# Kernel tuning notes

Measured on AMD Instinct MI355X. Metric: run time of the kernel, lower is better.

## Reference

```python
import jax, jax.numpy as jnp
import numpy as np

K = 30           # k for kNN graph in each DynamicEdgeConv
NS = 0.2         # LeakyReLU negative_slope used by the repo's MLP
N = 16384        # number of points
E = 262144       # number of candidate edges
IN_CH = 3


def _glorot(key, shape):
    fan_in, fan_out = shape
    s = jnp.sqrt(6.0 / (fan_in + fan_out))
    return jax.random.uniform(key, shape, minval=-s, maxval=s, dtype=jnp.float32)


def setup_inputs() -> dict:
    key = jax.random.key(0)
    ks = jax.random.split(key, 8)
    x = jax.random.normal(ks[0], (N, IN_CH), dtype=jnp.float32)
    edge_index = jax.random.randint(ks[1], (2, E), 0, N)
    return {
        "x": x,
        "edge_index": edge_index,
        # conv1: MLP([2*in_ch, 64])
        "W1": _glorot(ks[2], (2 * IN_CH, 64)), "b1": jnp.zeros((64,), jnp.float32),
        # conv2/conv3: MLP([2*64, 64])
        "W2": _glorot(ks[3], (128, 64)), "b2": jnp.zeros((64,), jnp.float32),
        "W3": _glorot(ks[4], (128, 64)), "b3": jnp.zeros((64,), jnp.float32),
        # edge head W = MLP([2*64, 64, 1])
        "Wh1": _glorot(ks[5], (128, 64)), "bh1": jnp.zeros((64,), jnp.float32),
        "Wh2": _glorot(ks[6], (64, 1)), "bh2": jnp.zeros((1,), jnp.float32),
    }


def _knn_idx(x, k):
    # kNN in feature space (includes self, as PyG's knn(x, x, k) does)
    sq = jnp.sum(x * x, axis=1)                       # [N]
    d = sq[:, None] + sq[None, :] - 2.0 * (x @ x.T)   # [N, N] squared distances
    return jax.lax.top_k(-d, k)[1]                    # [N, k]


def _edge_conv(x, W, b):
    # DynamicEdgeConv: per-neighbor MLP on [x_i, x_j - x_i], max aggregation
    idx = _knn_idx(x, K)                              # [N, K]
    xj = x[idx]                                       # [N, K, C]
    xi = jnp.broadcast_to(x[:, None, :], xj.shape)
    feat = jnp.concatenate([xi, xj - xi], axis=-1)    # [N, K, 2C]
    h = jax.nn.leaky_relu(feat @ W + b, NS)           # [N, K, 64]
    return jnp.max(h, axis=1)                         # [N, 64]


def reference(x, edge_index, W1, b1, W2, b2, W3, b3, Wh1, bh1, Wh2, bh2):
    x = _edge_conv(x, W1, b1)
    x = _edge_conv(x, W2, b2)
    x = _edge_conv(x, W3, b3)
    # torch.sort(edge_index, dim=0) canonicalizes each column (i<=j).
    # unique + inverse-gather is mathematically the identity on the per-edge
    # outputs (duplicate columns produce identical rows), so we compute the
    # edge head directly on the sorted (canonical) edges.
    v = jnp.sort(edge_index, axis=0)                  # [2, E]
    e = jnp.concatenate([x[v[0]], x[v[1]]], axis=1)   # [E, 128]
    h = jax.nn.leaky_relu(e @ Wh1 + bh1, NS)          # [E, 64]
    out = h @ Wh2 + bh2                               # [E, 1]
    return jax.nn.sigmoid(out).reshape(-1)            # [E]
```

## Files before the change

kernel.cpp:

```cpp
#include <hip/hip_runtime.h>
#include <cmath>

typedef __attribute__((ext_vector_type(8))) short bf16x8;
typedef __attribute__((ext_vector_type(4))) float f32x4;

constexpr int N_PTS = 16384;
constexpr int KK    = 30;
constexpr int NEDGE = 262144;
constexpr float NS  = 0.2f;
constexpr int S_SL  = 16;
constexpr int M_L   = 8;
constexpr int CPQ   = S_SL * 4 * M_L;

__device__ inline short f2bf_rne(float f) {
  unsigned u = __float_as_uint(f);
  unsigned r = (u + 0x7fffu + ((u >> 16) & 1u)) >> 16;
  return (short)r;
}

#define CEA(a, i, j) { unsigned lo_ = a[i] < a[j] ? a[i] : a[j]; \
                       unsigned hi_ = a[i] < a[j] ? a[j] : a[i]; \
                       a[i] = lo_; a[j] = hi_; }
#define SORT8(a) \
  CEA(a,0,1) CEA(a,2,3) CEA(a,4,5) CEA(a,6,7) \
  CEA(a,0,2) CEA(a,1,3) CEA(a,4,6) CEA(a,5,7) \
  CEA(a,1,2) CEA(a,5,6) \
  CEA(a,0,4) CEA(a,1,5) CEA(a,2,6) CEA(a,3,7) \
  CEA(a,2,4) CEA(a,3,5) \
  CEA(a,1,2) CEA(a,3,4) CEA(a,5,6)
#define MERGE8(kd, nk) \
  { _Pragma("unroll") for (int t_ = 0; t_ < 8; ++t_) { \
      unsigned v_ = nk[7 - t_]; kd[t_] = kd[t_] < v_ ? kd[t_] : v_; } } \
  CEA(kd,0,4) CEA(kd,1,5) CEA(kd,2,6) CEA(kd,3,7) \
  CEA(kd,0,2) CEA(kd,1,3) CEA(kd,4,6) CEA(kd,5,7) \
  CEA(kd,0,1) CEA(kd,2,3) CEA(kd,4,5) CEA(kd,6,7)

#define CEP(i, j) { bool c_ = (d[i] < d[j]) || (d[i] == d[j] && id[i] < id[j]); \
  float dl_ = c_ ? d[i] : d[j], dh_ = c_ ? d[j] : d[i]; \
  int   il_ = c_ ? id[i] : id[j], ih_ = c_ ? id[j] : id[i]; \
  d[i] = dl_; d[j] = dh_; id[i] = il_; id[j] = ih_; }
#define SORTP8() \
  CEP(0,1) CEP(2,3) CEP(4,5) CEP(6,7) \
  CEP(0,2) CEP(1,3) CEP(4,6) CEP(5,7) \
  CEP(1,2) CEP(5,6) \
  CEP(0,4) CEP(1,5) CEP(2,6) CEP(3,7) \
  CEP(2,4) CEP(3,5) \
  CEP(1,2) CEP(3,4) CEP(5,6)

#define ROR_ADD(x, N) \
  { float t_ = __int_as_float(__builtin_amdgcn_update_dpp( \
        0, __float_as_int(x), 0x120 + (N), 0xF, 0xF, 0)); (x) += t_; }

__global__ __launch_bounds__(256) void sq3(const float* __restrict__ X,
                                           float* __restrict__ sqv) {
  int p = blockIdx.x * 256 + threadIdx.x;
  float s = 0.f;
#pragma unroll
  for (int c = 0; c < 3; ++c) { float v = X[(size_t)p * 3 + c]; s = fmaf(v, v, s); }
  sqv[p] = s;
}

template<int C, int CP>
__global__ __launch_bounds__(256) void sqhi(const float* __restrict__ X,
    float* __restrict__ sqv, short* __restrict__ Xh) {
  int p = blockIdx.x * 256 + threadIdx.x;
  float s = 0.f;
#pragma unroll
  for (int c = 0; c < C; ++c) {
    float v = X[(size_t)p * C + c];
    s = fmaf(v, v, s);
    Xh[(size_t)p * CP + c] = f2bf_rne(v);
  }
#pragma unroll
  for (int c = C; c < CP; ++c) Xh[(size_t)p * CP + c] = 0;
  sqv[p] = s;
}

__global__ __launch_bounds__(256) void knn_scan3(
    const float* __restrict__ X, const float* __restrict__ sqv,
    unsigned short* __restrict__ cand) {
  const int q = blockIdx.x * 256 + threadIdx.x;
  const int slice = blockIdx.y;
  const int c0 = slice * 1024;
  const float x0 = X[(size_t)q * 3 + 0];
  const float x1 = X[(size_t)q * 3 + 1];
  const float x2 = X[(size_t)q * 3 + 2];

  unsigned kq0[8], kq1[8], kq2[8], kq3[8];
#pragma unroll
  for (int t = 0; t < 8; ++t) { kq0[t]=0xFFFFFFFFu; kq1[t]=0xFFFFFFFFu;
                                kq2[t]=0xFFFFFFFFu; kq3[t]=0xFFFFFFFFu; }

#define SCAN_QTR(kd, QO) \
  for (int t = 0; t < 256; t += 8) { \
    unsigned nk[8]; \
    _Pragma("unroll") for (int u = 0; u < 8; ++u) { \
      const int j = c0 + (QO) * 256 + t + u; \
      float dj = fmaf(x0, X[(size_t)j*3+0], fmaf(x1, X[(size_t)j*3+1], x2 * X[(size_t)j*3+2])); \
      float key = fmaf(dj, -2.f, sqv[j]); \
      unsigned uu = __float_as_uint(key); \
      uu ^= ((unsigned)((int)uu >> 31)) | 0x80000000u; \
      nk[u] = (uu & 0xFFFFFF00u) | (unsigned)(t + u); \
    } \
    SORT8(nk) MERGE8(kd, nk) \
  }
  SCAN_QTR(kq0, 0)
  SCAN_QTR(kq1, 1)
  SCAN_QTR(kq2, 2)
  SCAN_QTR(kq3, 3)
#undef SCAN_QTR

  unsigned short* o = cand + (size_t)q * CPQ + slice * 32;
#pragma unroll
  for (int t = 0; t < 8; ++t) {
    o[t]      = (unsigned short)(c0 +   0 + (int)(kq0[t] & 0xFFu));
    o[8 + t]  = (unsigned short)(c0 + 256 + (int)(kq1[t] & 0xFFu));
    o[16 + t] = (unsigned short)(c0 + 512 + (int)(kq2[t] & 0xFFu));
    o[24 + t] = (unsigned short)(c0 + 768 + (int)(kq3[t] & 0xFFu));
  }
}

template<int KT>
__global__ __launch_bounds__(256) void knn_pass1(
    const short* __restrict__ Xh, const float* __restrict__ sqv,
    unsigned short* __restrict__ cand) {
  constexpr int CP = KT * 32;
  const int tid  = threadIdx.x;
  const int lane = tid & 63;
  const int wv   = tid >> 6;
  const int col  = lane & 15;
  const int quad = lane >> 4;
  const int qb   = blockIdx.x * 256 + wv * 64 + col;
  const int slice = blockIdx.y;
  const int slen = N_PTS / S_SL;
  const int c0 = slice * slen;

  bf16x8 bq[4][KT];
#pragma unroll
  for (int g = 0; g < 4; ++g)
#pragma unroll
    for (int kt = 0; kt < KT; ++kt)
      bq[g][kt] = *(const bf16x8*)(Xh + (size_t)(qb + g * 16) * CP + kt * 32 + quad * 8);

  unsigned kd0[M_L], kd1[M_L], kd2[M_L], kd3[M_L];
#pragma unroll
  for (int t = 0; t < M_L; ++t) {
    kd0[t] = 0xFFFFFFFFu; kd1[t] = 0xFFFFFFFFu;
    kd2[t] = 0xFFFFFFFFu; kd3[t] = 0xFFFFFFFFu;
  }

  const int NB = slen / 32;
  for (int bt = 0; bt < NB; ++bt) {
    const int cb = c0 + bt * 32;
    const size_t arow0 = (size_t)(cb + col) * CP + quad * 8;
    const size_t arow1 = arow0 + (size_t)16 * CP;
    unsigned nk0[8], nk1[8], nk2[8], nk3[8];
    {
      bf16x8 ah[KT];
#pragma unroll
      for (int kt = 0; kt < KT; ++kt)
        ah[kt] = *(const bf16x8*)(Xh + arow0 + kt * 32);
      f32x4 a0 = {0.f,0.f,0.f,0.f}, a1 = {0.f,0.f,0.f,0.f};
      f32x4 a2 = {0.f,0.f,0.f,0.f}, a3 = {0.f,0.f,0.f,0.f};
#pragma unroll
      for (int kt = 0; kt < KT; ++kt) {
        a0 = __builtin_amdgcn_mfma_f32_16x16x32_bf16(ah[kt], bq[0][kt], a0, 0, 0, 0);
        a1 = __builtin_amdgcn_mfma_f32_16x16x32_bf16(ah[kt], bq[1][kt], a1, 0, 0, 0);
        a2 = __builtin_amdgcn_mfma_f32_16x16x32_bf16(ah[kt], bq[2][kt], a2, 0, 0, 0);
        a3 = __builtin_amdgcn_mfma_f32_16x16x32_bf16(ah[kt], bq[3][kt], a3, 0, 0, 0);
      }
      f32x4 sc = *(const f32x4*)(sqv + cb + quad * 4);
      const unsigned lb = (unsigned)bt * 8;
#pragma unroll
      for (int r = 0; r < 4; ++r) {
        unsigned u0 = __float_as_uint(fmaf(a0[r], -2.f, sc[r]));
        unsigned u1 = __float_as_uint(fmaf(a1[r], -2.f, sc[r]));
        unsigned u2 = __float_as_uint(fmaf(a2[r], -2.f, sc[r]));
        unsigned u3 = __float_as_uint(fmaf(a3[r], -2.f, sc[r]));
        u0 ^= ((unsigned)((int)u0 >> 31)) | 0x80000000u;
        u1 ^= ((unsigned)((int)u1 >> 31)) | 0x80000000u;
        u2 ^= ((unsigned)((int)u2 >> 31)) | 0x80000000u;
        u3 ^= ((unsigned)((int)u3 >> 31)) | 0x80000000u;
        nk0[r] = (u0 & 0xFFFFFF00u) | (lb + r);
        nk1[r] = (u1 & 0xFFFFFF00u) | (lb + r);
        nk2[r] = (u2 & 0xFFFFFF00u) | (lb + r);
        nk3[r] = (u3 & 0xFFFFFF00u) | (lb + r);
      }
    }
    {
      bf16x8 ah[KT];
#pragma unroll
      for (int kt = 0; kt < KT; ++kt)
        ah[kt] = *(const bf16x8*)(Xh + arow1 + kt * 32);
      f32x4 a0 = {0.f,0.f,0.f,0.f}, a1 = {0.f,0.f,0.f,0.f};
      f32x4 a2 = {0.f,0.f,0.f,0.f}, a3 = {0.f,0.f,0.f,0.f};
#pragma unroll
      for (int kt = 0; kt < KT; ++kt) {
        a0 = __builtin_amdgcn_mfma_f32_16x16x32_bf16(ah[kt], bq[0][kt], a0, 0, 0, 0);
        a1 = __builtin_amdgcn_mfma_f32_16x16x32_bf16(ah[kt], bq[1][kt], a1, 0, 0, 0);
        a2 = __builtin_amdgcn_mfma_f32_16x16x32_bf16(ah[kt], bq[2][kt], a2, 0, 0, 0);
        a3 = __builtin_amdgcn_mfma_f32_16x16x32_bf16(ah[kt], bq[3][kt], a3, 0, 0, 0);
      }
      f32x4 sc = *(const f32x4*)(sqv + cb + 16 + quad * 4);
      const unsigned lb = (unsigned)bt * 8 + 4;
#pragma unroll
      for (int r = 0; r < 4; ++r) {
        unsigned u0 = __float_as_uint(fmaf(a0[r], -2.f, sc[r]));
        unsigned u1 = __float_as_uint(fmaf(a1[r], -2.f, sc[r]));
        unsigned u2 = __float_as_uint(fmaf(a2[r], -2.f, sc[r]));
        unsigned u3 = __float_as_uint(fmaf(a3[r], -2.f, sc[r]));
        u0 ^= ((unsigned)((int)u0 >> 31)) | 0x80000000u;
        u1 ^= ((unsigned)((int)u1 >> 31)) | 0x80000000u;
        u2 ^= ((unsigned)((int)u2 >> 31)) | 0x80000000u;
        u3 ^= ((unsigned)((int)u3 >> 31)) | 0x80000000u;
        nk0[4 + r] = (u0 & 0xFFFFFF00u) | (lb + r);
        nk1[4 + r] = (u1 & 0xFFFFFF00u) | (lb + r);
        nk2[4 + r] = (u2 & 0xFFFFFF00u) | (lb + r);
        nk3[4 + r] = (u3 & 0xFFFFFF00u) | (lb + r);
      }
    }
    SORT8(nk0) MERGE8(kd0, nk0)
    SORT8(nk1) MERGE8(kd1, nk1)
    SORT8(nk2) MERGE8(kd2, nk2)
    SORT8(nk3) MERGE8(kd3, nk3)
  }

#pragma unroll
  for (int g = 0; g < 4; ++g) {
    const unsigned* kd = (g == 0) ? kd0 : (g == 1) ? kd1 : (g == 2) ? kd2 : kd3;
    unsigned short* o =
        cand + ((size_t)(qb + g * 16) * S_SL + slice) * (4 * M_L) + quad * M_L;
#pragma unroll
    for (int t = 0; t < M_L; ++t) {
      unsigned l = kd[t] & 0xFFu;
      o[t] = (unsigned short)(c0 + (int)(l >> 2) * 16 + quad * 4 + (int)(l & 3));
    }
  }
}

__global__ __launch_bounds__(256) void knn_pass2v2(
    const float* __restrict__ X, const float* __restrict__ sqv,
    const unsigned short* __restrict__ cand, int* __restrict__ knn) {
  __shared__ int   ldsC[4][CPQ];
  __shared__ float ldsD[4][CPQ];
  const int lane = threadIdx.x & 63, wv = threadIdx.x >> 6;
  const int q = blockIdx.x * 4 + wv;
  const int s = lane & 15;
  const int g = lane >> 4;
  const float sqq = sqv[q];
  constexpr int PL = CPQ / 64;

#pragma unroll
  for (int u = 0; u < PL; ++u)
    ldsC[wv][u * 64 + lane] = (int)cand[(size_t)q * CPQ + u * 64 + lane];
  f32x4 xq = *(const f32x4*)(X + (size_t)q * 64 + s * 4);
  __syncthreads();

  for (int it = 0; it < CPQ / 16; ++it) {
    int jj[4];
#pragma unroll
    for (int uu = 0; uu < 4; ++uu) jj[uu] = ldsC[wv][it * 16 + uu * 4 + g];
    f32x4 vv[4];
#pragma unroll
    for (int uu = 0; uu < 4; ++uu)
      vv[uu] = *(const f32x4*)(X + (size_t)jj[uu] * 64 + s * 4);
    float sj[4];
#pragma unroll
    for (int uu = 0; uu < 4; ++uu) sj[uu] = sqv[jj[uu]];
#pragma unroll
    for (int uu = 0; uu < 4; ++uu) {
      float p = fmaf(xq[0], vv[uu][0], fmaf(xq[1], vv[uu][1],
                fmaf(xq[2], vv[uu][2], xq[3] * vv[uu][3])));
      ROR_ADD(p, 8) ROR_ADD(p, 4) ROR_ADD(p, 2) ROR_ADD(p, 1)
      if (s == 0) ldsD[wv][it * 16 + uu * 4 + g] = (sqq + sj[uu]) - 2.f * p;
    }
  }
  __syncthreads();

  float d[PL]; int id[PL];
#pragma unroll
  for (int u = 0; u < PL; ++u) {
    d[u]  = ldsD[wv][u * 64 + lane];
    id[u] = ldsC[wv][u * 64 + lane];
  }
  SORTP8();
  for (int r = 0; r < KK; ++r) {
    float bd = d[0]; int bi = id[0];
#pragma unroll
    for (int off = 32; off; off >>= 1) {
      float od = __shfl_xor(bd, off, 64);
      int   oi = __shfl_xor(bi, off, 64);
      bool c = (od < bd) || (od == bd && oi < bi);
      bd = c ? od : bd; bi = c ? oi : bi;
    }
    if (lane == 0) knn[(size_t)q * KK + r] = bi;
    bool win = (d[0] == bd) && (id[0] == bi);
#pragma unroll
    for (int t = 0; t < PL - 1; ++t) {
      d[t]  = win ? d[t + 1]  : d[t];
      id[t] = win ? id[t + 1] : id[t];
    }
    d[PL - 1] = win ? __builtin_inff() : d[PL - 1];
  }
}

template<int C, int GRP, int LG>
__global__ __launch_bounds__(256) void knn_pass2co(
    const float* __restrict__ X, const float* __restrict__ sqv,
    const unsigned short* __restrict__ cand, int* __restrict__ knn) {
  __shared__ float ldsD[4][CPQ];
  const int lane = threadIdx.x & 63, wv = threadIdx.x >> 6;
  const int q = blockIdx.x * 4 + wv;
  const int s = lane & (GRP - 1);
  const int g = lane >> LG;
  constexpr int RPI = 64 / GRP;
  constexpr int NIT = CPQ / RPI;
  const float sqq = sqv[q];

  float xqv[4];
  if constexpr (GRP == 16) {
#pragma unroll
    for (int u = 0; u < 4; ++u) xqv[u] = X[(size_t)q * C + s * 4 + u];
  } else {
    xqv[0] = (s < C) ? X[(size_t)q * C + s] : 0.f;
  }

  for (int it = 0; it < NIT; ++it) {
    const int t = it * RPI + g;
    const int j = (int)cand[(size_t)q * CPQ + t];
    float p;
    if constexpr (GRP == 16) {
      f32x4 v = *(const f32x4*)(X + (size_t)j * C + s * 4);
      p = fmaf(xqv[0], v[0], fmaf(xqv[1], v[1], fmaf(xqv[2], v[2], xqv[3] * v[3])));
    } else {
      float v = (s < C) ? X[(size_t)j * C + s] : 0.f;
      p = xqv[0] * v;
    }
#pragma unroll
    for (int off = 1; off < GRP; off <<= 1) p += __shfl_xor(p, off, 64);
    if (s == 0) ldsD[wv][t] = (sqq + sqv[j]) - 2.f * p;
  }
  __syncthreads();

  constexpr int PL = CPQ / 64;
  float d[PL]; int id[PL];
#pragma unroll
  for (int u = 0; u < PL; ++u) {
    d[u]  = ldsD[wv][u * 64 + lane];
    id[u] = (int)cand[(size_t)q * CPQ + u * 64 + lane];
  }
  for (int r = 0; r < KK; ++r) {
    float bd = d[0]; int bi = id[0];
#pragma unroll
    for (int u = 1; u < PL; ++u) {
      bool c = (d[u] < bd) || (d[u] == bd && id[u] < bi);
      bd = c ? d[u] : bd; bi = c ? id[u] : bi;
    }
#pragma unroll
    for (int off = 32; off; off >>= 1) {
      float od = __shfl_xor(bd, off, 64);
      int   oi = __shfl_xor(bi, off, 64);
      bool c = (od < bd) || (od == bd && oi < bi);
      bd = c ? od : bd; bi = c ? oi : bi;
    }
    if (lane == 0) knn[(size_t)q * KK + r] = bi;
#pragma unroll
    for (int u = 0; u < PL; ++u) if (id[u] == bi) d[u] = __builtin_inff();
  }
}

template<int C, int PPW>
__global__ __launch_bounds__(256) void edge_conv(
    const float* __restrict__ X, const int* __restrict__ knn,
    const float* __restrict__ W, const float* __restrict__ B,
    float* __restrict__ Y) {
  const int wv = __builtin_amdgcn_readfirstlane(threadIdx.x >> 6);
  const int lane = threadIdx.x & 63;
  float wd[C], wj[C];
#pragma unroll
  for (int c = 0; c < C; ++c) {
    float w0 = W[c * 64 + lane];
    float w1 = W[(C + c) * 64 + lane];
    wd[c] = w0 - w1; wj[c] = w1;
  }
  const float bb = B[lane];
  const int p0 = (blockIdx.x * 4 + wv) * PPW;
  for (int pp = 0; pp < PPW; ++pp) {
    const int p = p0 + pp;
    const float* __restrict__ xi = X + (size_t)p * C;
    float base = bb;
#pragma unroll
    for (int c = 0; c < C; ++c) base = fmaf(xi[c], wd[c], base);
    float m = -__builtin_inff();
    for (int n = 0; n < KK; ++n) {
      const int j = __builtin_amdgcn_readfirstlane(knn[(size_t)p * KK + n]);
      const float* __restrict__ xj = X + (size_t)j * C;
      float acc;
      if constexpr (C % 4 == 0) {
        float a0 = 0.f, a1 = 0.f, a2 = 0.f, a3 = 0.f;
#pragma unroll
        for (int c = 0; c < C; c += 4) {
          a0 = fmaf(xj[c + 0], wj[c + 0], a0);
          a1 = fmaf(xj[c + 1], wj[c + 1], a1);
          a2 = fmaf(xj[c + 2], wj[c + 2], a2);
          a3 = fmaf(xj[c + 3], wj[c + 3], a3);
        }
        acc = base + ((a0 + a1) + (a2 + a3));
      } else {
        acc = base;
#pragma unroll
        for (int c = 0; c < C; ++c) acc = fmaf(xj[c], wj[c], acc);
      }
      acc = acc > 0.f ? acc : NS * acc;
      m = fmaxf(m, acc);
    }
    Y[(size_t)p * 64 + lane] = m;
  }
}

template<int EPW>
__global__ __launch_bounds__(256) void edge_head(
    const float* __restrict__ X, const int* __restrict__ ei,
    const float* __restrict__ Wh1, const float* __restrict__ bh1,
    const float* __restrict__ Wh2, const float* __restrict__ bh2,
    float* __restrict__ out) {
  const int wv = __builtin_amdgcn_readfirstlane(threadIdx.x >> 6);
  const int lane = threadIdx.x & 63;
  float w0[64], w1[64];
#pragma unroll
  for (int c = 0; c < 64; ++c) {
    w0[c] = Wh1[c * 64 + lane];
    w1[c] = Wh1[(64 + c) * 64 + lane];
  }
  const float bb = bh1[lane];
  const float wv2 = Wh2[lane];
  const float b2 = bh2[0];
  const int e0 = (blockIdx.x * 4 + wv) * EPW;
  for (int ee = 0; ee < EPW; ++ee) {
    const int e = e0 + ee;
    const int a = ei[e], b = ei[NEDGE + e];
    const int v0 = __builtin_amdgcn_readfirstlane(min(a, b));
    const int v1 = __builtin_amdgcn_readfirstlane(max(a, b));
    const float* __restrict__ f0 = X + (size_t)v0 * 64;
    const float* __restrict__ f1 = X + (size_t)v1 * 64;
    float a0 = 0.f, a1 = 0.f, a2 = 0.f, a3 = 0.f;
#pragma unroll
    for (int c = 0; c < 64; c += 4) {
      a0 = fmaf(f0[c + 0], w0[c + 0], a0);
      a1 = fmaf(f0[c + 1], w0[c + 1], a1);
      a2 = fmaf(f0[c + 2], w0[c + 2], a2);
      a3 = fmaf(f0[c + 3], w0[c + 3], a3);
    }
#pragma unroll
    for (int c = 0; c < 64; c += 4) {
      a0 = fmaf(f1[c + 0], w1[c + 0], a0);
      a1 = fmaf(f1[c + 1], w1[c + 1], a1);
      a2 = fmaf(f1[c + 2], w1[c + 2], a2);
      a3 = fmaf(f1[c + 3], w1[c + 3], a3);
    }
    float h = bb + ((a0 + a1) + (a2 + a3));
    h = h > 0.f ? h : NS * h;
    float z = h * wv2;
#pragma unroll
    for (int off = 32; off; off >>= 1) z += __shfl_xor(z, off, 64);
    if (lane == 0) out[e] = 1.f / (1.f + expf(-(z + b2)));
  }
}

extern "C" void kernel_launch(void* const* d_in, const int* in_sizes, int n_in,
                              void* d_out, int out_size, void* d_ws, size_t ws_size,
                              hipStream_t stream) {
  const float* x   = (const float*)d_in[0];
  const int*   ei  = (const int*)d_in[1];
  const float* W1  = (const float*)d_in[2];
  const float* b1  = (const float*)d_in[3];
  const float* W2  = (const float*)d_in[4];
  const float* b2  = (const float*)d_in[5];
  const float* W3  = (const float*)d_in[6];
  const float* b3  = (const float*)d_in[7];
  const float* Wh1 = (const float*)d_in[8];
  const float* bh1 = (const float*)d_in[9];
  const float* Wh2 = (const float*)d_in[10];
  const float* bh2 = (const float*)d_in[11];
  float* out = (float*)d_out;

  char* ws = (char*)d_ws;
  float* xA  = (float*)ws; ws += (size_t)N_PTS * 64 * 4;
  float* xB  = (float*)ws; ws += (size_t)N_PTS * 64 * 4;
  float* sqb = (float*)ws; ws += (size_t)N_PTS * 4;
  int*   knn = (int*)ws;   ws += (size_t)N_PTS * KK * 4;
  short* Xh  = (short*)ws; ws += (size_t)N_PTS * 64 * 2;
  unsigned short* cand = (unsigned short*)ws;
  ws += (size_t)N_PTS * CPQ * 2;
  (void)ws_size; (void)in_sizes; (void)n_in; (void)out_size;

  sq3<<<N_PTS / 256, 256, 0, stream>>>(x, sqb);
  knn_scan3<<<dim3(N_PTS / 256, S_SL), 256, 0, stream>>>(x, sqb, cand);
  knn_pass2co<3, 4, 2><<<N_PTS / 4, 256, 0, stream>>>(x, sqb, cand, knn);
  edge_conv<3, 4><<<N_PTS / 16, 256, 0, stream>>>(x, knn, W1, b1, xA);
  sqhi<64, 64><<<N_PTS / 256, 256, 0, stream>>>(xA, sqb, Xh);
  knn_pass1<2><<<dim3(N_PTS / 256, S_SL), 256, 0, stream>>>(Xh, sqb, cand);
  knn_pass2v2<<<N_PTS / 4, 256, 0, stream>>>(xA, sqb, cand, knn);
  edge_conv<64, 4><<<N_PTS / 16, 256, 0, stream>>>(xA, knn, W2, b2, xB);
  sqhi<64, 64><<<N_PTS / 256, 256, 0, stream>>>(xB, sqb, Xh);
  knn_pass1<2><<<dim3(N_PTS / 256, S_SL), 256, 0, stream>>>(Xh, sqb, cand);
  knn_pass2v2<<<N_PTS / 4, 256, 0, stream>>>(xB, sqb, cand, knn);
  edge_conv<64, 4><<<N_PTS / 16, 256, 0, stream>>>(xB, knn, W3, b3, xA);
  edge_head<16><<<NEDGE / 64, 256, 0, stream>>>(xA, ei, Wh1, bh1, Wh2, bh2, out);
}
```

Measured before the change: 1.208 ms.

## Run edge head on bf16 MFMA with hi/lo split for fp32 accuracy

Replaces the scalar-FMA edge-head MLP, which handled one edge per wave, with a matrix-core version. Each wave processes 16 edges per tile using 16x16x32 bf16 MFMAs, with features and weights split into bf16 high and low parts (three products) to approximate fp32 accuracy. Two small prep kernels build the split features and the pre-swizzled weight fragments. This adds two extra launches and workspace traffic, and gives slightly different rounding than fp32.

```diff
diff --git a/kernel.cpp b/kernel.cpp
--- a/kernel.cpp
+++ b/kernel.cpp
@@ -76,6 +76,33 @@
   sqv[p] = s;
 }
 
+__global__ __launch_bounds__(256) void xsplit64(const float* __restrict__ X,
+    short* __restrict__ Xh, short* __restrict__ Xl) {
+  int i = blockIdx.x * 256 + threadIdx.x;
+  float v = X[i];
+  short h = f2bf_rne(v);
+  float hf = __uint_as_float(((unsigned)(unsigned short)h) << 16);
+  Xh[i] = h;
+  Xl[i] = f2bf_rne(v - hf);
+}
+
+__global__ __launch_bounds__(256) void wh1prep(const float* __restrict__ Wh1,
+    short* __restrict__ whH, short* __restrict__ whL) {
+  for (int i = threadIdx.x; i < 1024; i += 256) {
+    int lane = i & 63, ktct = i >> 6;
+    int kt = ktct & 3, ct = ktct >> 2;
+    int colw = lane & 15, quadw = lane >> 4;
+#pragma unroll
+    for (int j = 0; j < 8; ++j) {
+      float v = Wh1[(size_t)(kt * 32 + quadw * 8 + j) * 64 + ct * 16 + colw];
+      short h = f2bf_rne(v);
+      float hf = __uint_as_float(((unsigned)(unsigned short)h) << 16);
+      whH[(size_t)i * 8 + j] = h;
+      whL[(size_t)i * 8 + j] = f2bf_rne(v - hf);
+    }
+  }
+}
+
 __global__ __launch_bounds__(256) void knn_scan3(
     const float* __restrict__ X, const float* __restrict__ sqv,
     unsigned short* __restrict__ cand) {
@@ -418,52 +445,75 @@
   }
 }
 
-template<int EPW>
-__global__ __launch_bounds__(256) void edge_head(
-    const float* __restrict__ X, const int* __restrict__ ei,
-    const float* __restrict__ Wh1, const float* __restrict__ bh1,
-    const float* __restrict__ Wh2, const float* __restrict__ bh2,
-    float* __restrict__ out) {
-  const int wv = __builtin_amdgcn_readfirstlane(threadIdx.x >> 6);
-  const int lane = threadIdx.x & 63;
-  float w0[64], w1[64];
-#pragma unroll
-  for (int c = 0; c < 64; ++c) {
-    w0[c] = Wh1[c * 64 + lane];
-    w1[c] = Wh1[(64 + c) * 64 + lane];
-  }
-  const float bb = bh1[lane];
-  const float wv2 = Wh2[lane];
+template<int ET>
+__global__ __launch_bounds__(256) void edge_head_mfma(
+    const short* __restrict__ Xh, const short* __restrict__ Xl,
+    const int* __restrict__ ei,
+    const short* __restrict__ whH, const short* __restrict__ whL,
+    const float* __restrict__ bh1, const float* __restrict__ Wh2,
+    const float* __restrict__ bh2, float* __restrict__ out) {
+  const int lane = threadIdx.x & 63, wv = threadIdx.x >> 6;
+  const int col = lane & 15, quad = lane >> 4;
+
+  bf16x8 bh[4][4], bl[4][4];
+#pragma unroll
+  for (int ct = 0; ct < 4; ++ct)
+#pragma unroll
+    for (int kt = 0; kt < 4; ++kt) {
+      const size_t idx = ((size_t)(ct * 4 + kt) * 64 + lane) * 8;
+      bh[ct][kt] = *(const bf16x8*)(whH + idx);
+      bl[ct][kt] = *(const bf16x8*)(whL + idx);
+    }
+  float bb[4], w2[4];
+#pragma unroll
+  for (int ct = 0; ct < 4; ++ct) {
+    bb[ct] = bh1[ct * 16 + col];
+    w2[ct] = Wh2[ct * 16 + col];
+  }
   const float b2 = bh2[0];
-  const int e0 = (blockIdx.x * 4 + wv) * EPW;
-  for (int ee = 0; ee < EPW; ++ee) {
-    const int e = e0 + ee;
+
+  const int t0 = (blockIdx.x * 4 + wv) * ET;
+  for (int tt = 0; tt < ET; ++tt) {
+    const int e = (t0 + tt) * 16 + col;
     const int a = ei[e], b = ei[NEDGE + e];
-    const int v0 = __builtin_amdgcn_readfirstlane(min(a, b));
-    const int v1 = __builtin_amdgcn_readfirstlane(max(a, b));
-    const float* __restrict__ f0 = X + (size_t)v0 * 64;
-    const float* __restrict__ f1 = X + (size_t)v1 * 64;
-    float a0 = 0.f, a1 = 0.f, a2 = 0.f, a3 = 0.f;
-#pragma unroll
-    for (int c = 0; c < 64; c += 4) {
-      a0 = fmaf(f0[c + 0], w0[c + 0], a0);
-      a1 = fmaf(f0[c + 1], w0[c + 1], a1);
-      a2 = fmaf(f0[c + 2], w0[c + 2], a2);
-      a3 = fmaf(f0[c + 3], w0[c + 3], a3);
-    }
-#pragma unroll
-    for (int c = 0; c < 64; c += 4) {
-      a0 = fmaf(f1[c + 0], w1[c + 0], a0);
-      a1 = fmaf(f1[c + 1], w1[c + 1], a1);
-      a2 = fmaf(f1[c + 2], w1[c + 2], a2);
-      a3 = fmaf(f1[c + 3], w1[c + 3], a3);
-    }
-    float h = bb + ((a0 + a1) + (a2 + a3));
-    h = h > 0.f ? h : NS * h;
-    float z = h * wv2;
-#pragma unroll
-    for (int off = 32; off; off >>= 1) z += __shfl_xor(z, off, 64);
-    if (lane == 0) out[e] = 1.f / (1.f + expf(-(z + b2)));
+    const int v0 = min(a, b), v1 = max(a, b);
+    bf16x8 ah[4], al[4];
+#pragma unroll
+    for (int kt = 0; kt < 4; ++kt) {
+      const int row = (kt < 2) ? v0 : v1;
+      const size_t off = (size_t)row * 64 + (kt & 1) * 32 + quad * 8;
+      ah[kt] = *(const bf16x8*)(Xh + off);
+      al[kt] = *(const bf16x8*)(Xl + off);
+    }
+    f32x4 acc[4];
+#pragma unroll
+    for (int ct = 0; ct < 4; ++ct) acc[ct] = f32x4{0.f, 0.f, 0.f, 0.f};
+#pragma unroll
+    for (int kt = 0; kt < 4; ++kt)
+#pragma unroll
+      for (int ct = 0; ct < 4; ++ct) {
+        acc[ct] = __builtin_amdgcn_mfma_f32_16x16x32_bf16(ah[kt], bh[ct][kt], acc[ct], 0, 0, 0);
+        acc[ct] = __builtin_amdgcn_mfma_f32_16x16x32_bf16(ah[kt], bl[ct][kt], acc[ct], 0, 0, 0);
+        acc[ct] = __builtin_amdgcn_mfma_f32_16x16x32_bf16(al[kt], bh[ct][kt], acc[ct], 0, 0, 0);
+      }
+    float z[4];
+#pragma unroll
+    for (int r = 0; r < 4; ++r) {
+      float zz = 0.f;
+#pragma unroll
+      for (int ct = 0; ct < 4; ++ct) {
+        float h = acc[ct][r] + bb[ct];
+        h = h > 0.f ? h : NS * h;
+        zz = fmaf(h, w2[ct], zz);
+      }
+      ROR_ADD(zz, 8) ROR_ADD(zz, 4) ROR_ADD(zz, 2) ROR_ADD(zz, 1)
+      z[r] = zz;
+    }
+    if (col == 0) {
+#pragma unroll
+      for (int r = 0; r < 4; ++r)
+        out[(t0 + tt) * 16 + quad * 4 + r] = 1.f / (1.f + expf(-(z[r] + b2)));
+    }
   }
 }
 
@@ -490,9 +540,14 @@
   float* sqb = (float*)ws; ws += (size_t)N_PTS * 4;
   int*   knn = (int*)ws;   ws += (size_t)N_PTS * KK * 4;
   short* Xh  = (short*)ws; ws += (size_t)N_PTS * 64 * 2;
+  short* Xl  = (short*)ws; ws += (size_t)N_PTS * 64 * 2;
+  short* whH = (short*)ws; ws += (size_t)8192 * 2;
+  short* whL = (short*)ws; ws += (size_t)8192 * 2;
   unsigned short* cand = (unsigned short*)ws;
   ws += (size_t)N_PTS * CPQ * 2;
   (void)ws_size; (void)in_sizes; (void)n_in; (void)out_size;
+
+  wh1prep<<<1, 256, 0, stream>>>(Wh1, whH, whL);
 
   sq3<<<N_PTS / 256, 256, 0, stream>>>(x, sqb);
   knn_scan3<<<dim3(N_PTS / 256, S_SL), 256, 0, stream>>>(x, sqb, cand);
@@ -506,5 +561,7 @@
   knn_pass1<2><<<dim3(N_PTS / 256, S_SL), 256, 0, stream>>>(Xh, sqb, cand);
   knn_pass2v2<<<N_PTS / 4, 256, 0, stream>>>(xB, sqb, cand, knn);
   edge_conv<64, 4><<<N_PTS / 16, 256, 0, stream>>>(xB, knn, W3, b3, xA);
-  edge_head<16><<<NEDGE / 64, 256, 0, stream>>>(xA, ei, Wh1, bh1, Wh2, bh2, out);
-}
+  xsplit64<<<(N_PTS * 64) / 256, 256, 0, stream>>>(xA, Xh, Xl);
+  edge_head_mfma<8><<<NEDGE / (16 * 4 * 8), 256, 0, stream>>>(
+      Xh, Xl, ei, whH, whL, bh1, Wh2, bh2, out);
+}
```

After: 1.087 ms. 10.0% less time.
